# Kernel optimization log

Measured on AMD Instinct MI355X. Metric: run time of the kernel, lower is better.

## Reference

```python
import jax, jax.numpy as jnp
import numpy as np

B, S, D, E, L = 8, 512, 768, 768, 4000

def setup_inputs() -> dict:
    key = jax.random.key(0)
    k1, k2, k3, k4 = jax.random.split(key, 4)
    last_hidden_state = jax.random.normal(k1, (B, S, D), dtype=jnp.float32)
    label_feat = jax.random.normal(k2, (L, E), dtype=jnp.float32)
    # nn.Linear(D, E): weight [E, D], bias [E]; xavier-ish scale
    W = jax.random.normal(k3, (E, D), dtype=jnp.float32) * (1.0 / np.sqrt(D))
    bias = jax.random.normal(k4, (E,), dtype=jnp.float32) * 0.01
    return {"last_hidden_state": last_hidden_state, "label_feat": label_feat, "W": W, "bias": bias}

def reference(last_hidden_state, label_feat, W, bias):
    # proj: tanh(Linear(last_hidden_state))  -> [B, S, E]
    proj = jnp.tanh(jnp.einsum('bsd,ed->bse', last_hidden_state, W) + bias)
    # scores: bmm(label_feat [B,L,E], proj^T [B,E,S]) -> [B, L, S]
    scores = jnp.einsum('le,bse->bls', label_feat, proj)
    # softmax over dim=1 (the LABEL dim), as in the original
    weights = jax.nn.softmax(scores, axis=1)
    # attn: bmm(weights [B,L,S], last_hidden_state [B,S,D]) -> [B, L, D]
    attn_output = jnp.einsum('bls,bsd->bld', weights, last_hidden_state)
    return (weights, attn_output)
```

## Files before the change

kernel.cpp:

```cpp
#include <hip/hip_runtime.h>
#include <hip/hip_bf16.h>
#include <cmath>

typedef __attribute__((ext_vector_type(8))) short short8;
typedef __attribute__((ext_vector_type(4))) float f32x4;

#define SM_CH 32

__device__ inline ushort f2bf(float x) {
    union { float f; unsigned u; } v; v.f = x;
    unsigned r = v.u + 0x7FFF + ((v.u >> 16) & 1);
    return (ushort)(r >> 16);
}

__device__ inline void split2(float x, ushort& hi, ushort& lo) {
    union { float f; unsigned u; } v; v.f = x;
    hi = (ushort)(v.u >> 16);
    union { float f; unsigned u; } h; h.u = v.u & 0xFFFF0000u;
    union { float f; unsigned u; } d; d.f = x - h.f;
    lo = (ushort)(d.u >> 16);
}

__device__ inline int swz(int row, int byte_in_row) {
    return row * 128 + (byte_in_row ^ ((row & 7) << 4));
}

__device__ inline void gload16(const void* g, void* lds) {
    __builtin_amdgcn_global_load_lds(
        (const __attribute__((address_space(1))) unsigned int*)g,
        (__attribute__((address_space(3))) unsigned int*)lds, 16, 0, 0);
}

__device__ inline void xcd_remap(int& bx, int& by, int& bz) {
    unsigned nx = gridDim.x, ny = gridDim.y;
    unsigned nwg = nx * ny * gridDim.z;
    unsigned id = blockIdx.x + nx * (blockIdx.y + ny * blockIdx.z);
    unsigned q = nwg >> 3;
    unsigned s = (id & 7) * q + (id >> 3);
    bx = s % nx; unsigned r = s / nx;
    by = r % ny; bz = r / ny;
}

__global__ __launch_bounds__(256) void split_planes_kernel(
    const float* __restrict__ in, ushort* __restrict__ H,
    ushort* __restrict__ L, long long n4)
{
    long long i = (long long)blockIdx.x * 256 + threadIdx.x;
    if (i >= n4) return;
    float4 v = *(const float4*)(in + i * 4);
    ushort h[4], l[4];
    split2(v.x, h[0], l[0]); split2(v.y, h[1], l[1]);
    split2(v.z, h[2], l[2]); split2(v.w, h[3], l[3]);
    *(ushort4*)(H + i * 4) = *(ushort4*)h;
    *(ushort4*)(L + i * 4) = *(ushort4*)l;
}

__global__ __launch_bounds__(256) void mfma_proj(
    const float* __restrict__ Ab, const float* __restrict__ Bb,
    ushort* __restrict__ CH, ushort* __restrict__ CL,
    const float* __restrict__ bias, int M, int N, int K)
{
    extern __shared__ char smem[];
    char* Ah = smem;
    char* Al = smem + 16384;
    char* Bh = smem + 32768;
    char* Bl = smem + 49152;

    int bx, by, bz; xcd_remap(bx, by, bz);
    const int bm = bx * 128;
    const int bn = by * 128;

    const int t  = threadIdx.x;
    const int srow = t >> 1;
    const int skh  = (t & 1) * 32;
    const float* ap = Ab + (long long)min(bm + srow, M - 1) * K + skh;
    const float* bp = Bb + (long long)min(bn + srow, N - 1) * K + skh;

    const int lane = t & 63;
    const int w    = t >> 6;
    const int wm   = (w >> 1) * 64;
    const int wn   = (w & 1) * 64;
    const int lrow = lane & 15;
    const int kg16 = (lane >> 4) * 16;

    f32x4 acc[4][4] = {};

    for (int k0 = 0; k0 < K; k0 += 64) {
        #pragma unroll
        for (int j = 0; j < 4; ++j) {
            float xs[8];
            *(float4*)&xs[0] = *(const float4*)(ap + k0 + j * 8);
            *(float4*)&xs[4] = *(const float4*)(ap + k0 + j * 8 + 4);
            ushort oh[8], ol[8];
            #pragma unroll
            for (int i = 0; i < 8; ++i) split2(xs[i], oh[i], ol[i]);
            const int off = swz(srow, skh * 2 + j * 16);
            *(uint4*)(Ah + off) = *(uint4*)oh;
            *(uint4*)(Al + off) = *(uint4*)ol;
        }
        #pragma unroll
        for (int j = 0; j < 4; ++j) {
            float xs[8];
            *(float4*)&xs[0] = *(const float4*)(bp + k0 + j * 8);
            *(float4*)&xs[4] = *(const float4*)(bp + k0 + j * 8 + 4);
            ushort oh[8], ol[8];
            #pragma unroll
            for (int i = 0; i < 8; ++i) split2(xs[i], oh[i], ol[i]);
            const int off = swz(srow, skh * 2 + j * 16);
            *(uint4*)(Bh + off) = *(uint4*)oh;
            *(uint4*)(Bl + off) = *(uint4*)ol;
        }
        __syncthreads();

        #pragma unroll
        for (int kk = 0; kk < 2; ++kk) {
            short8 ah[4], al[4];
            #pragma unroll
            for (int mi = 0; mi < 4; ++mi) {
                const int off = swz(wm + mi * 16 + lrow, kk * 64 + kg16);
                ah[mi] = *(const short8*)(Ah + off);
                al[mi] = *(const short8*)(Al + off);
            }
            #pragma unroll
            for (int ni = 0; ni < 4; ++ni) {
                const int off = swz(wn + ni * 16 + lrow, kk * 64 + kg16);
                short8 bh = *(const short8*)(Bh + off);
                short8 bl = *(const short8*)(Bl + off);
                #pragma unroll
                for (int mi = 0; mi < 4; ++mi) {
                    acc[mi][ni] = __builtin_amdgcn_mfma_f32_16x16x32_bf16(al[mi], bh, acc[mi][ni], 0, 0, 0);
                    acc[mi][ni] = __builtin_amdgcn_mfma_f32_16x16x32_bf16(ah[mi], bl, acc[mi][ni], 0, 0, 0);
                    acc[mi][ni] = __builtin_amdgcn_mfma_f32_16x16x32_bf16(ah[mi], bh, acc[mi][ni], 0, 0, 0);
                }
            }
        }
        __syncthreads();
    }

    const int r0 = bm + wm + (lane >> 4) * 4;
    const int c0 = bn + wn + (lane & 15);
    #pragma unroll
    for (int ni = 0; ni < 4; ++ni) {
        const int col = c0 + ni * 16;
        const float bv = bias[col];
        #pragma unroll
        for (int mi = 0; mi < 4; ++mi) {
            #pragma unroll
            for (int r = 0; r < 4; ++r) {
                const int row = r0 + mi * 16 + r;
                if (row < M) {
                    float x = tanhf(acc[mi][ni][r] + bv);
                    ushort h, l;
                    split2(x, h, l);
                    CH[(long long)row * N + col] = h;
                    CL[(long long)row * N + col] = l;
                }
            }
        }
    }
}

__global__ __launch_bounds__(256) void mfma_scores_pre(
    const ushort* __restrict__ AHb, const ushort* __restrict__ ALb,
    const ushort* __restrict__ BHb, const ushort* __restrict__ BLb,
    float* __restrict__ Cb, float* __restrict__ pmo, float* __restrict__ pso,
    int M, int N, int K, long long sB, long long sC)
{
    extern __shared__ char smem[];
    char* Ah = smem;
    char* Al = smem + 16384;
    char* Bh = smem + 32768;
    char* Bl = smem + 49152;

    int bx, by, bz; xcd_remap(bx, by, bz);
    const int bm = bx * 128;
    const int bn = by * 128;
    const long long z = bz;

    const ushort* BH = BHb + z * sB;
    const ushort* BL = BLb + z * sB;

    const int t    = threadIdx.x;
    const int lane = t & 63;
    const int w    = t >> 6;

    const int lr  = lane >> 3;
    const int lc8 = 8 * ((lane & 7) ^ lr);
    const ushort *ah_src[4], *al_src[4], *bh_src[4], *bl_src[4];
    int ldsO[4];
    #pragma unroll
    for (int i = 0; i < 4; ++i) {
        const int row = w * 32 + i * 8 + lr;
        ah_src[i] = AHb + (long long)min(bm + row, M - 1) * K + lc8;
        al_src[i] = ALb + (long long)min(bm + row, M - 1) * K + lc8;
        bh_src[i] = BH  + (long long)(bn + row) * K + lc8;
        bl_src[i] = BL  + (long long)(bn + row) * K + lc8;
        ldsO[i] = w * 4096 + i * 1024;
    }

    const int wm   = (w >> 1) * 64;
    const int wn   = (w & 1) * 64;
    const int lrow = lane & 15;
    const int kg16 = (lane >> 4) * 16;

    f32x4 acc[4][4] = {};

    for (int k0 = 0; k0 < K; k0 += 64) {
        #pragma unroll
        for (int i = 0; i < 4; ++i) {
            gload16(ah_src[i] + k0, Ah + ldsO[i]);
            gload16(al_src[i] + k0, Al + ldsO[i]);
            gload16(bh_src[i] + k0, Bh + ldsO[i]);
            gload16(bl_src[i] + k0, Bl + ldsO[i]);
        }
        __syncthreads();

        #pragma unroll
        for (int kk = 0; kk < 2; ++kk) {
            short8 ah[4], al[4];
            #pragma unroll
            for (int mi = 0; mi < 4; ++mi) {
                const int off = swz(wm + mi * 16 + lrow, kk * 64 + kg16);
                ah[mi] = *(const short8*)(Ah + off);
                al[mi] = *(const short8*)(Al + off);
            }
            #pragma unroll
            for (int ni = 0; ni < 4; ++ni) {
                const int off = swz(wn + ni * 16 + lrow, kk * 64 + kg16);
                short8 bh = *(const short8*)(Bh + off);
                short8 bl = *(const short8*)(Bl + off);
                #pragma unroll
                for (int mi = 0; mi < 4; ++mi) {
                    acc[mi][ni] = __builtin_amdgcn_mfma_f32_16x16x32_bf16(al[mi], bh, acc[mi][ni], 0, 0, 0);
                    acc[mi][ni] = __builtin_amdgcn_mfma_f32_16x16x32_bf16(ah[mi], bl, acc[mi][ni], 0, 0, 0);
                    acc[mi][ni] = __builtin_amdgcn_mfma_f32_16x16x32_bf16(ah[mi], bh, acc[mi][ni], 0, 0, 0);
                }
            }
        }
        __syncthreads();
    }

    float* C = Cb + z * sC;
    const int r0 = bm + wm + (lane >> 4) * 4;
    const int c0 = bn + wn + (lane & 15);
    #pragma unroll
    for (int ni = 0; ni < 4; ++ni) {
        const int col = c0 + ni * 16;
        #pragma unroll
        for (int mi = 0; mi < 4; ++mi) {
            #pragma unroll
            for (int r = 0; r < 4; ++r) {
                const int row = r0 + mi * 16 + r;
                if (row < M) C[(long long)row * N + col] = acc[mi][ni][r];
            }
        }
    }

    float* red = (float*)smem;
    const int slot = ((w >> 1) << 2) | (lane >> 4);
    const int colb = wn + (lane & 15);

    float lm[4];
    #pragma unroll
    for (int ni = 0; ni < 4; ++ni) {
        float v = -INFINITY;
        #pragma unroll
        for (int mi = 0; mi < 4; ++mi)
            #pragma unroll
            for (int r = 0; r < 4; ++r)
                if (r0 + mi * 16 + r < M) v = fmaxf(v, acc[mi][ni][r]);
        lm[ni] = v;
    }
    #pragma unroll
    for (int ni = 0; ni < 4; ++ni)
        red[(colb + ni * 16) * 8 + slot] = lm[ni];
    __syncthreads();
    float cm[4];
    #pragma unroll
    for (int ni = 0; ni < 4; ++ni) {
        float v = -INFINITY;
        #pragma unroll
        for (int s8 = 0; s8 < 8; ++s8)
            v = fmaxf(v, red[(colb + ni * 16) * 8 + s8]);
        cm[ni] = v;
    }
    __syncthreads();
    float ls[4];
    #pragma unroll
    for (int ni = 0; ni < 4; ++ni) {
        float sum = 0.f;
        #pragma unroll
        for (int mi = 0; mi < 4; ++mi)
            #pragma unroll
            for (int r = 0; r < 4; ++r)
                if (r0 + mi * 16 + r < M) sum += __expf(acc[mi][ni][r] - cm[ni]);
        ls[ni] = sum;
    }
    #pragma unroll
    for (int ni = 0; ni < 4; ++ni)
        red[(colb + ni * 16) * 8 + slot] = ls[ni];
    __syncthreads();
    if (slot == 0) {
        #pragma unroll
        for (int ni = 0; ni < 4; ++ni) {
            float sum = 0.f;
            #pragma unroll
            for (int s8 = 0; s8 < 8; ++s8)
                sum += red[(colb + ni * 16) * 8 + s8];
            const int col = bn + colb + ni * 16;
            pmo[(z * SM_CH + bx) * N + col] = cm[ni];
            pso[(z * SM_CH + bx) * N + col] = sum;
        }
    }
}

__global__ __launch_bounds__(256) void mfma_attn2(
    const ushort* __restrict__ Ab, const ushort* __restrict__ Bb,
    float* __restrict__ Cb, int M, int N, int K,
    long long sA, long long sB, long long sC)
{
    extern __shared__ char smem[];
    char* Ah = smem;
    char* Bh = smem + 16384;

    int bx, by, bz; xcd_remap(bx, by, bz);
    const int bm = bx * 128;
    const int bn = by * 256;
    const long long z = bz;

    const ushort* A = Ab + z * sA;
    const ushort* B = Bb + z * sB;

    const int t    = threadIdx.x;
    const int lane = t & 63;
    const int w    = t >> 6;

    const int lr  = lane >> 3;
    const int lc8 = 8 * ((lane & 7) ^ lr);
    const ushort* a_src[4];
    int ldsA[4];
    #pragma unroll
    for (int i = 0; i < 4; ++i) {
        const int row = w * 32 + i * 8 + lr;
        a_src[i] = A + (long long)min(bm + row, M - 1) * K + lc8;
        ldsA[i] = w * 4096 + i * 1024;
    }
    const ushort* b_src[8];
    int ldsB[8];
    #pragma unroll
    for (int i = 0; i < 8; ++i) {
        const int row = w * 64 + i * 8 + lr;
        b_src[i] = B + (long long)(bn + row) * K + lc8;
        ldsB[i] = w * 8192 + i * 1024;
    }

    const int wm   = (w >> 1) * 64;
    const int wn   = (w & 1) * 128;
    const int lrow = lane & 15;
    const int kg16 = (lane >> 4) * 16;

    f32x4 acc[4][8] = {};

    for (int k0 = 0; k0 < K; k0 += 64) {
        #pragma unroll
        for (int i = 0; i < 4; ++i)
            gload16(a_src[i] + k0, Ah + ldsA[i]);
        #pragma unroll
        for (int i = 0; i < 8; ++i)
            gload16(b_src[i] + k0, Bh + ldsB[i]);
        __syncthreads();

        #pragma unroll
        for (int kk = 0; kk < 2; ++kk) {
            short8 ah[4];
            #pragma unroll
            for (int mi = 0; mi < 4; ++mi)
                ah[mi] = *(const short8*)(Ah + swz(wm + mi * 16 + lrow, kk * 64 + kg16));
            #pragma unroll
            for (int ni = 0; ni < 8; ++ni) {
                short8 bh = *(const short8*)(Bh + swz(wn + ni * 16 + lrow, kk * 64 + kg16));
                #pragma unroll
                for (int mi = 0; mi < 4; ++mi)
                    acc[mi][ni] = __builtin_amdgcn_mfma_f32_16x16x32_bf16(ah[mi], bh, acc[mi][ni], 0, 0, 0);
            }
        }
        __syncthreads();
    }

    float* C = Cb + z * sC;
    const int r0 = bm + wm + (lane >> 4) * 4;
    const int c0 = bn + wn + (lane & 15);
    #pragma unroll
    for (int ni = 0; ni < 8; ++ni) {
        const int col = c0 + ni * 16;
        #pragma unroll
        for (int mi = 0; mi < 4; ++mi) {
            #pragma unroll
            for (int r = 0; r < 4; ++r) {
                const int row = r0 + mi * 16 + r;
                if (row < M) C[(long long)row * N + col] = acc[mi][ni][r];
            }
        }
    }
}

__global__ __launch_bounds__(256) void transpose_bf16_kernel(
    const float* __restrict__ in, ushort* __restrict__ out, int S, int D)
{
    __shared__ float tile[32][33];
    const int b = blockIdx.z;
    const int s0 = blockIdx.x * 32, d0 = blockIdx.y * 32;
    const int tx = threadIdx.x & 31, ty = threadIdx.x >> 5;
    const float* ip = in + (long long)b * S * D;
    #pragma unroll
    for (int i = 0; i < 32; i += 8)
        tile[ty + i][tx] = ip[(long long)(s0 + ty + i) * D + d0 + tx];
    __syncthreads();
    ushort* op = out + (long long)b * S * D;
    #pragma unroll
    for (int i = 0; i < 32; i += 8)
        op[(long long)(d0 + ty + i) * S + s0 + tx] = f2bf(tile[tx][ty + i]);
}

__global__ __launch_bounds__(256) void softmax_merge_kernel(
    const float* __restrict__ pm, const float* __restrict__ ps,
    float* __restrict__ fm, float* __restrict__ fsinv, int S)
{
    int s = blockIdx.x * 256 + threadIdx.x;
    int b = blockIdx.y;
    float m = -INFINITY;
    #pragma unroll
    for (int c = 0; c < SM_CH; ++c)
        m = fmaxf(m, pm[(b * SM_CH + c) * S + s]);
    float sum = 0.f;
    #pragma unroll
    for (int c = 0; c < SM_CH; ++c)
        sum += ps[(b * SM_CH + c) * S + s] * __expf(pm[(b * SM_CH + c) * S + s] - m);
    fm[b * S + s] = m;
    fsinv[b * S + s] = 1.f / sum;
}

__global__ __launch_bounds__(256) void softmax_write_kernel(
    float* __restrict__ scores, const float* __restrict__ fm,
    const float* __restrict__ fsinv, int L, int S, int chlen,
    ushort* __restrict__ wbf)
{
    int s = blockIdx.x * 256 + threadIdx.x;
    int c = blockIdx.y;
    int b = blockIdx.z;
    float m   = fm[b * S + s];
    float inv = fsinv[b * S + s];
    float* p = scores + (long long)b * L * S + s;
    ushort* q = wbf + (long long)b * L * S + s;
    int l0 = c * chlen;
    int l1 = min(L, l0 + chlen);
    for (int l = l0; l < l1; ++l) {
        float x = p[(long long)l * S];
        float v = __expf(x - m) * inv;
        p[(long long)l * S] = v;
        q[(long long)l * S] = f2bf(v);
    }
}

extern "C" void kernel_launch(void* const* d_in, const int* in_sizes, int n_in,
                              void* d_out, int out_size, void* d_ws, size_t ws_size,
                              hipStream_t stream)
{
    const int Bn = 8, S = 512, D = 768, E = 768, L = 4000;
    const float* lhs   = (const float*)d_in[0];
    const float* label = (const float*)d_in[1];
    const float* W     = (const float*)d_in[2];
    const float* bias  = (const float*)d_in[3];

    float* weights = (float*)d_out;
    float* attn    = (float*)d_out + (long long)Bn * L * S;

    const long long nLE  = (long long)L * E;
    const long long nBSE = (long long)Bn * S * E;
    const long long nBDS = (long long)Bn * D * S;
    const long long nBLS = (long long)Bn * L * S;

    ushort* labelH = (ushort*)d_ws;
    ushort* labelL = labelH + nLE;
    ushort* projH  = labelL + nLE;
    ushort* projL  = projH + nBSE;
    ushort* lhsT   = projL + nBSE;
    ushort* wbf    = lhsT + nBDS;
    float*  pm     = (float*)(wbf + nBLS);
    float*  ps     = pm + Bn * SM_CH * S;
    float*  fm     = ps + Bn * SM_CH * S;
    float*  fsinv  = fm + Bn * S;

    const int chlen = (L + SM_CH - 1) / SM_CH;

    transpose_bf16_kernel<<<dim3(S / 32, D / 32, Bn), 256, 0, stream>>>(
        lhs, lhsT, S, D);
    split_planes_kernel<<<(int)(nLE / 4 + 255) / 256, 256, 0, stream>>>(
        label, labelH, labelL, nLE / 4);

    mfma_proj<<<dim3((Bn * S) / 128, E / 128, 1), 256, 65536, stream>>>(
        lhs, W, projH, projL, bias, Bn * S, E, D);

    mfma_scores_pre<<<dim3((L + 127) / 128, S / 128, Bn), 256, 65536, stream>>>(
        labelH, labelL, projH, projL, weights, pm, ps, L, S, E,
        (long long)S * E, (long long)L * S);

    softmax_merge_kernel<<<dim3(S / 256, Bn), 256, 0, stream>>>(
        pm, ps, fm, fsinv, S);
    softmax_write_kernel<<<dim3(S / 256, SM_CH, Bn), 256, 0, stream>>>(
        weights, fm, fsinv, L, S, chlen, wbf);

    mfma_attn2<<<dim3((L + 127) / 128, D / 256, Bn), 256, 49152, stream>>>(
        wbf, lhsT, attn, L, D, S,
        (long long)L * S, (long long)D * S, (long long)L * D);
}
```

Measured before the change: 265.3 us.

## Replace scores and attention GEMMs with a double-buffered 512-thread MFMA template

```diff
diff --git a/kernel.cpp b/kernel.cpp
--- a/kernel.cpp
+++ b/kernel.cpp
@@ -5,7 +5,8 @@
 typedef __attribute__((ext_vector_type(8))) short short8;
 typedef __attribute__((ext_vector_type(4))) float f32x4;
 
-#define SM_CH 32
+#define SM_CH 16
+#define WCH   32
 
 __device__ inline ushort f2bf(float x) {
     union { float f; unsigned u; } v; v.f = x;
@@ -39,6 +40,202 @@
     unsigned s = (id & 7) * q + (id >> 3);
     bx = s % nx; unsigned r = s / nx;
     by = r % ny; bz = r / ny;
+}
+
+template<int ROWS, int KS>
+__device__ inline void stage_plane(const ushort* __restrict__ src,
+                                   char* plane, int t, int rbase, int rmax)
+{
+    #pragma unroll
+    for (int s = 0; s < ROWS / 64; ++s) {
+        const int row = s * 64 + (t >> 3);
+        const int col = (((t & 7) * 16) ^ ((row & 7) << 4)) >> 1;
+        const int gr  = min(rbase + row, rmax);
+        gload16(src + (long long)gr * KS + col,
+                plane + s * 8192 + (t >> 6) * 1024);
+    }
+}
+
+template<bool SPLIT3, int BM, int MREP, bool STATS, int NT, int KS, int VMN>
+__global__ __launch_bounds__(512, 2) void mfma8(
+    const ushort* __restrict__ AH, const ushort* __restrict__ AL,
+    const ushort* __restrict__ BH, const ushort* __restrict__ BL,
+    float* __restrict__ Cb, float* __restrict__ pmo, float* __restrict__ pso,
+    int M, int N, long long sA, long long sB, long long sC)
+{
+    extern __shared__ char smem[];
+    constexpr int ABYTES = BM * 128;
+
+    int bx, by, bz; xcd_remap(bx, by, bz);
+    const int bm = bx * BM;
+    const int bn = by * 256;
+    const long long z = bz;
+
+    const ushort* AHb = AH + z * sA;
+    const ushort* ALb = SPLIT3 ? (AL + z * sA) : AHb;
+    const ushort* BHb = BH + z * sB;
+    const ushort* BLb = SPLIT3 ? (BL + z * sB) : BHb;
+
+    const int t    = threadIdx.x;
+    const int lane = t & 63;
+    const int w    = t >> 6;
+    const int wr   = w >> 2;
+    const int wc   = w & 3;
+    const int lrow = lane & 15;
+    const int kg16 = (lane >> 4) * 16;
+
+    const ushort* Ap; const ushort* Bp; int kc;
+#define SELPLANES(tt_)                                                        \
+    do {                                                                      \
+        if constexpr (SPLIT3) {                                               \
+            Ap = ((tt_) < 24) ? AHb : ALb;                                    \
+            Bp = (((tt_) < 12) || ((tt_) >= 24)) ? BHb : BLb;                 \
+            int seg_ = ((tt_) < 12) ? (tt_) : (((tt_) < 24) ? (tt_) - 12      \
+                                                            : (tt_) - 24);   \
+            kc = seg_ * 64;                                                   \
+        } else { Ap = AHb; Bp = BHb; kc = (tt_) * 64; }                       \
+    } while (0)
+
+    SELPLANES(0);
+    stage_plane<BM, KS>(Ap + kc, smem, t, bm, M - 1);
+    stage_plane<256, KS>(Bp + kc, smem + 2 * ABYTES, t, bn, N - 1);
+    SELPLANES(1);
+    stage_plane<BM, KS>(Ap + kc, smem + ABYTES, t, bm, M - 1);
+    stage_plane<256, KS>(Bp + kc, smem + 2 * ABYTES + 32768, t, bn, N - 1);
+    if constexpr (VMN == 8) asm volatile("s_waitcnt vmcnt(8)" ::: "memory");
+    else                    asm volatile("s_waitcnt vmcnt(6)" ::: "memory");
+    __builtin_amdgcn_s_barrier();
+
+    f32x4 acc[MREP][4] = {};
+
+    for (int tt = 0; tt < NT; ++tt) {
+        const int cur = tt & 1;
+        char* Ab = smem + cur * ABYTES;
+        char* Bb = smem + 2 * ABYTES + cur * 32768;
+
+        __builtin_amdgcn_s_setprio(1);
+        short8 bf[4][2];
+        #pragma unroll
+        for (int n = 0; n < 4; ++n)
+            #pragma unroll
+            for (int ks = 0; ks < 2; ++ks)
+                bf[n][ks] = *(const short8*)(Bb + swz(wc * 64 + n * 16 + lrow,
+                                                      ks * 64 + kg16));
+        #pragma unroll
+        for (int q = 0; q < MREP / 2; ++q) {
+            short8 af[2][2];
+            #pragma unroll
+            for (int mi = 0; mi < 2; ++mi)
+                #pragma unroll
+                for (int ks = 0; ks < 2; ++ks)
+                    af[mi][ks] = *(const short8*)(Ab +
+                        swz(wr * (BM / 2) + (q * 2 + mi) * 16 + lrow,
+                            ks * 64 + kg16));
+            #pragma unroll
+            for (int ks = 0; ks < 2; ++ks)
+                #pragma unroll
+                for (int mi = 0; mi < 2; ++mi)
+                    #pragma unroll
+                    for (int n = 0; n < 4; ++n)
+                        acc[q * 2 + mi][n] = __builtin_amdgcn_mfma_f32_16x16x32_bf16(
+                            af[mi][ks], bf[n][ks], acc[q * 2 + mi][n], 0, 0, 0);
+        }
+        __builtin_amdgcn_s_setprio(0);
+
+        asm volatile("s_waitcnt lgkmcnt(0)" ::: "memory");
+        __builtin_amdgcn_s_barrier();
+
+        if (tt + 2 < NT) {
+            SELPLANES(tt + 2);
+            stage_plane<BM, KS>(Ap + kc, smem + cur * ABYTES, t, bm, M - 1);
+            stage_plane<256, KS>(Bp + kc, smem + 2 * ABYTES + cur * 32768,
+                                 t, bn, N - 1);
+            if constexpr (VMN == 8)
+                asm volatile("s_waitcnt vmcnt(8)" ::: "memory");
+            else
+                asm volatile("s_waitcnt vmcnt(6)" ::: "memory");
+        } else {
+            asm volatile("s_waitcnt vmcnt(0)" ::: "memory");
+        }
+        __builtin_amdgcn_s_barrier();
+    }
+#undef SELPLANES
+
+    float* C = Cb + z * sC;
+    const int r0 = bm + wr * (BM / 2) + (lane >> 4) * 4;
+    const int c0 = bn + wc * 64 + (lane & 15);
+    #pragma unroll
+    for (int n = 0; n < 4; ++n) {
+        const int col = c0 + n * 16;
+        #pragma unroll
+        for (int mi = 0; mi < MREP; ++mi) {
+            #pragma unroll
+            for (int r = 0; r < 4; ++r) {
+                const int row = r0 + mi * 16 + r;
+                if (row < M) C[(long long)row * N + col] = acc[mi][n][r];
+            }
+        }
+    }
+
+    if constexpr (STATS) {
+        __syncthreads();
+        float* red = (float*)smem;
+        const int slot = wr * 4 + (lane >> 4);
+        const int colb = wc * 64 + (lane & 15);
+
+        float lm[4];
+        #pragma unroll
+        for (int n = 0; n < 4; ++n) {
+            float v = -INFINITY;
+            #pragma unroll
+            for (int mi = 0; mi < MREP; ++mi)
+                #pragma unroll
+                for (int r = 0; r < 4; ++r)
+                    if (r0 + mi * 16 + r < M) v = fmaxf(v, acc[mi][n][r]);
+            lm[n] = v;
+        }
+        #pragma unroll
+        for (int n = 0; n < 4; ++n)
+            red[(colb + n * 16) * 8 + slot] = lm[n];
+        __syncthreads();
+        float cm[4];
+        #pragma unroll
+        for (int n = 0; n < 4; ++n) {
+            float v = -INFINITY;
+            #pragma unroll
+            for (int s8 = 0; s8 < 8; ++s8)
+                v = fmaxf(v, red[(colb + n * 16) * 8 + s8]);
+            cm[n] = v;
+        }
+        __syncthreads();
+        float ls[4];
+        #pragma unroll
+        for (int n = 0; n < 4; ++n) {
+            float sum = 0.f;
+            #pragma unroll
+            for (int mi = 0; mi < MREP; ++mi)
+                #pragma unroll
+                for (int r = 0; r < 4; ++r)
+                    if (r0 + mi * 16 + r < M) sum += __expf(acc[mi][n][r] - cm[n]);
+            ls[n] = sum;
+        }
+        #pragma unroll
+        for (int n = 0; n < 4; ++n)
+            red[(colb + n * 16) * 8 + slot] = ls[n];
+        __syncthreads();
+        if (slot == 0) {
+            #pragma unroll
+            for (int n = 0; n < 4; ++n) {
+                float sum = 0.f;
+                #pragma unroll
+                for (int s8 = 0; s8 < 8; ++s8)
+                    sum += red[(colb + n * 16) * 8 + s8];
+                const int col = bn + colb + n * 16;
+                pmo[(z * SM_CH + bx) * N + col] = cm[n];
+                pso[(z * SM_CH + bx) * N + col] = sum;
+            }
+        }
+    }
 }
 
 __global__ __launch_bounds__(256) void split_planes_kernel(
@@ -155,250 +352,6 @@
                     CH[(long long)row * N + col] = h;
                     CL[(long long)row * N + col] = l;
                 }
-            }
-        }
-    }
-}
-
-__global__ __launch_bounds__(256) void mfma_scores_pre(
-    const ushort* __restrict__ AHb, const ushort* __restrict__ ALb,
-    const ushort* __restrict__ BHb, const ushort* __restrict__ BLb,
-    float* __restrict__ Cb, float* __restrict__ pmo, float* __restrict__ pso,
-    int M, int N, int K, long long sB, long long sC)
-{
-    extern __shared__ char smem[];
-    char* Ah = smem;
-    char* Al = smem + 16384;
-    char* Bh = smem + 32768;
-    char* Bl = smem + 49152;
-
-    int bx, by, bz; xcd_remap(bx, by, bz);
-    const int bm = bx * 128;
-    const int bn = by * 128;
-    const long long z = bz;
-
-    const ushort* BH = BHb + z * sB;
-    const ushort* BL = BLb + z * sB;
-
-    const int t    = threadIdx.x;
-    const int lane = t & 63;
-    const int w    = t >> 6;
-
-    const int lr  = lane >> 3;
-    const int lc8 = 8 * ((lane & 7) ^ lr);
-    const ushort *ah_src[4], *al_src[4], *bh_src[4], *bl_src[4];
-    int ldsO[4];
-    #pragma unroll
-    for (int i = 0; i < 4; ++i) {
-        const int row = w * 32 + i * 8 + lr;
-        ah_src[i] = AHb + (long long)min(bm + row, M - 1) * K + lc8;
-        al_src[i] = ALb + (long long)min(bm + row, M - 1) * K + lc8;
-        bh_src[i] = BH  + (long long)(bn + row) * K + lc8;
-        bl_src[i] = BL  + (long long)(bn + row) * K + lc8;
-        ldsO[i] = w * 4096 + i * 1024;
-    }
-
-    const int wm   = (w >> 1) * 64;
-    const int wn   = (w & 1) * 64;
-    const int lrow = lane & 15;
-    const int kg16 = (lane >> 4) * 16;
-
-    f32x4 acc[4][4] = {};
-
-    for (int k0 = 0; k0 < K; k0 += 64) {
-        #pragma unroll
-        for (int i = 0; i < 4; ++i) {
-            gload16(ah_src[i] + k0, Ah + ldsO[i]);
-            gload16(al_src[i] + k0, Al + ldsO[i]);
-            gload16(bh_src[i] + k0, Bh + ldsO[i]);
-            gload16(bl_src[i] + k0, Bl + ldsO[i]);
-        }
-        __syncthreads();
-
-        #pragma unroll
-        for (int kk = 0; kk < 2; ++kk) {
-            short8 ah[4], al[4];
-            #pragma unroll
-            for (int mi = 0; mi < 4; ++mi) {
-                const int off = swz(wm + mi * 16 + lrow, kk * 64 + kg16);
-                ah[mi] = *(const short8*)(Ah + off);
-                al[mi] = *(const short8*)(Al + off);
-            }
-            #pragma unroll
-            for (int ni = 0; ni < 4; ++ni) {
-                const int off = swz(wn + ni * 16 + lrow, kk * 64 + kg16);
-                short8 bh = *(const short8*)(Bh + off);
-                short8 bl = *(const short8*)(Bl + off);
-                #pragma unroll
-                for (int mi = 0; mi < 4; ++mi) {
-                    acc[mi][ni] = __builtin_amdgcn_mfma_f32_16x16x32_bf16(al[mi], bh, acc[mi][ni], 0, 0, 0);
-                    acc[mi][ni] = __builtin_amdgcn_mfma_f32_16x16x32_bf16(ah[mi], bl, acc[mi][ni], 0, 0, 0);
-                    acc[mi][ni] = __builtin_amdgcn_mfma_f32_16x16x32_bf16(ah[mi], bh, acc[mi][ni], 0, 0, 0);
-                }
-            }
-        }
-        __syncthreads();
-    }
-
-    float* C = Cb + z * sC;
-    const int r0 = bm + wm + (lane >> 4) * 4;
-    const int c0 = bn + wn + (lane & 15);
-    #pragma unroll
-    for (int ni = 0; ni < 4; ++ni) {
-        const int col = c0 + ni * 16;
-        #pragma unroll
-        for (int mi = 0; mi < 4; ++mi) {
-            #pragma unroll
-            for (int r = 0; r < 4; ++r) {
-                const int row = r0 + mi * 16 + r;
-                if (row < M) C[(long long)row * N + col] = acc[mi][ni][r];
-            }
-        }
-    }
-
-    float* red = (float*)smem;
-    const int slot = ((w >> 1) << 2) | (lane >> 4);
-    const int colb = wn + (lane & 15);
-
-    float lm[4];
-    #pragma unroll
-    for (int ni = 0; ni < 4; ++ni) {
-        float v = -INFINITY;
-        #pragma unroll
-        for (int mi = 0; mi < 4; ++mi)
-            #pragma unroll
-            for (int r = 0; r < 4; ++r)
-                if (r0 + mi * 16 + r < M) v = fmaxf(v, acc[mi][ni][r]);
-        lm[ni] = v;
-    }
-    #pragma unroll
-    for (int ni = 0; ni < 4; ++ni)
-        red[(colb + ni * 16) * 8 + slot] = lm[ni];
-    __syncthreads();
-    float cm[4];
-    #pragma unroll
-    for (int ni = 0; ni < 4; ++ni) {
-        float v = -INFINITY;
-        #pragma unroll
-        for (int s8 = 0; s8 < 8; ++s8)
-            v = fmaxf(v, red[(colb + ni * 16) * 8 + s8]);
-        cm[ni] = v;
-    }
-    __syncthreads();
-    float ls[4];
-    #pragma unroll
-    for (int ni = 0; ni < 4; ++ni) {
-        float sum = 0.f;
-        #pragma unroll
-        for (int mi = 0; mi < 4; ++mi)
-            #pragma unroll
-            for (int r = 0; r < 4; ++r)
-                if (r0 + mi * 16 + r < M) sum += __expf(acc[mi][ni][r] - cm[ni]);
-        ls[ni] = sum;
-    }
-    #pragma unroll
-    for (int ni = 0; ni < 4; ++ni)
-        red[(colb + ni * 16) * 8 + slot] = ls[ni];
-    __syncthreads();
-    if (slot == 0) {
-        #pragma unroll
-        for (int ni = 0; ni < 4; ++ni) {
-            float sum = 0.f;
-            #pragma unroll
-            for (int s8 = 0; s8 < 8; ++s8)
-                sum += red[(colb + ni * 16) * 8 + s8];
-            const int col = bn + colb + ni * 16;
-            pmo[(z * SM_CH + bx) * N + col] = cm[ni];
-            pso[(z * SM_CH + bx) * N + col] = sum;
-        }
-    }
-}
-
-__global__ __launch_bounds__(256) void mfma_attn2(
-    const ushort* __restrict__ Ab, const ushort* __restrict__ Bb,
-    float* __restrict__ Cb, int M, int N, int K,
-    long long sA, long long sB, long long sC)
-{
-    extern __shared__ char smem[];
-    char* Ah = smem;
-    char* Bh = smem + 16384;
-
-    int bx, by, bz; xcd_remap(bx, by, bz);
-    const int bm = bx * 128;
-    const int bn = by * 256;
-    const long long z = bz;
-
-    const ushort* A = Ab + z * sA;
-    const ushort* B = Bb + z * sB;
-
-    const int t    = threadIdx.x;
-    const int lane = t & 63;
-    const int w    = t >> 6;
-
-    const int lr  = lane >> 3;
-    const int lc8 = 8 * ((lane & 7) ^ lr);
-    const ushort* a_src[4];
-    int ldsA[4];
-    #pragma unroll
-    for (int i = 0; i < 4; ++i) {
-        const int row = w * 32 + i * 8 + lr;
-        a_src[i] = A + (long long)min(bm + row, M - 1) * K + lc8;
-        ldsA[i] = w * 4096 + i * 1024;
-    }
-    const ushort* b_src[8];
-    int ldsB[8];
-    #pragma unroll
-    for (int i = 0; i < 8; ++i) {
-        const int row = w * 64 + i * 8 + lr;
-        b_src[i] = B + (long long)(bn + row) * K + lc8;
-        ldsB[i] = w * 8192 + i * 1024;
-    }
-
-    const int wm   = (w >> 1) * 64;
-    const int wn   = (w & 1) * 128;
-    const int lrow = lane & 15;
-    const int kg16 = (lane >> 4) * 16;
-
-    f32x4 acc[4][8] = {};
-
-    for (int k0 = 0; k0 < K; k0 += 64) {
-        #pragma unroll
-        for (int i = 0; i < 4; ++i)
-            gload16(a_src[i] + k0, Ah + ldsA[i]);
-        #pragma unroll
-        for (int i = 0; i < 8; ++i)
-            gload16(b_src[i] + k0, Bh + ldsB[i]);
-        __syncthreads();
-
-        #pragma unroll
-        for (int kk = 0; kk < 2; ++kk) {
-            short8 ah[4];
-            #pragma unroll
-            for (int mi = 0; mi < 4; ++mi)
-                ah[mi] = *(const short8*)(Ah + swz(wm + mi * 16 + lrow, kk * 64 + kg16));
-            #pragma unroll
-            for (int ni = 0; ni < 8; ++ni) {
-                short8 bh = *(const short8*)(Bh + swz(wn + ni * 16 + lrow, kk * 64 + kg16));
-                #pragma unroll
-                for (int mi = 0; mi < 4; ++mi)
-                    acc[mi][ni] = __builtin_amdgcn_mfma_f32_16x16x32_bf16(ah[mi], bh, acc[mi][ni], 0, 0, 0);
-            }
-        }
-        __syncthreads();
-    }
-
-    float* C = Cb + z * sC;
-    const int r0 = bm + wm + (lane >> 4) * 4;
-    const int c0 = bn + wn + (lane & 15);
-    #pragma unroll
-    for (int ni = 0; ni < 8; ++ni) {
-        const int col = c0 + ni * 16;
-        #pragma unroll
-        for (int mi = 0; mi < 4; ++mi) {
-            #pragma unroll
-            for (int r = 0; r < 4; ++r) {
-                const int row = r0 + mi * 16 + r;
-                if (row < M) C[(long long)row * N + col] = acc[mi][ni][r];
             }
         }
     }
@@ -491,7 +444,12 @@
     float*  fm     = ps + Bn * SM_CH * S;
     float*  fsinv  = fm + Bn * S;
 
-    const int chlen = (L + SM_CH - 1) / SM_CH;
+    auto scoresK = mfma8<true, 256, 8, true, 36, 768, 8>;
+    auto attnK   = mfma8<false, 128, 4, false, 8, 512, 6>;
+    hipFuncSetAttribute((const void*)scoresK,
+                        hipFuncAttributeMaxDynamicSharedMemorySize, 131072);
+    hipFuncSetAttribute((const void*)attnK,
+                        hipFuncAttributeMaxDynamicSharedMemorySize, 98304);
 
     transpose_bf16_kernel<<<dim3(S / 32, D / 32, Bn), 256, 0, stream>>>(
         lhs, lhsT, S, D);
@@ -501,16 +459,16 @@
     mfma_proj<<<dim3((Bn * S) / 128, E / 128, 1), 256, 65536, stream>>>(
         lhs, W, projH, projL, bias, Bn * S, E, D);
 
-    mfma_scores_pre<<<dim3((L + 127) / 128, S / 128, Bn), 256, 65536, stream>>>(
-        labelH, labelL, projH, projL, weights, pm, ps, L, S, E,
-        (long long)S * E, (long long)L * S);
+    scoresK<<<dim3((L + 255) / 256, S / 256, Bn), 512, 131072, stream>>>(
+        labelH, labelL, projH, projL, weights, pm, ps,
+        L, S, 0LL, (long long)S * E, (long long)L * S);
 
     softmax_merge_kernel<<<dim3(S / 256, Bn), 256, 0, stream>>>(
         pm, ps, fm, fsinv, S);
-    softmax_write_kernel<<<dim3(S / 256, SM_CH, Bn), 256, 0, stream>>>(
-        weights, fm, fsinv, L, S, chlen, wbf);
-
-    mfma_attn2<<<dim3((L + 127) / 128, D / 256, Bn), 256, 49152, stream>>>(
-        wbf, lhsT, attn, L, D, S,
-        (long long)L * S, (long long)D * S, (long long)L * D);
-}
+    softmax_write_kernel<<<dim3(S / 256, WCH, Bn), 256, 0, stream>>>(
+        weights, fm, fsinv, L, S, (L + WCH - 1) / WCH, wbf);
+
+    attnK<<<dim3((L + 127) / 128, D / 256, Bn), 512, 98304, stream>>>(
+        wbf, nullptr, lhsT, nullptr, attn, nullptr, nullptr,
+        L, D, (long long)L * S, (long long)D * S, (long long)L * D);
+}
```

Result: faster. 250.8 us (-5.5%).
